# Kernel optimization log

Measured on AMD Instinct MI355X. Metric: run time of the kernel, lower is better.

The kernel has to match this reference:

```python
import jax, jax.numpy as jnp
import numpy as np

VOCAB = 128
HIDDEN = 1024

def setup_inputs() -> dict:
    key = jax.random.key(0)
    kx, ku, kw, kl, kb = jax.random.split(key, 5)
    B, S = 64, 512
    X = jax.random.randint(kx, (B, S), 0, VOCAB)
    # xavier_uniform bounds
    bu = float(np.sqrt(6.0 / (HIDDEN + HIDDEN)))
    bw = float(np.sqrt(6.0 / (HIDDEN + VOCAB)))
    U = jax.random.uniform(ku, (HIDDEN, HIDDEN), minval=-bu, maxval=bu, dtype=jnp.float32)
    W = jax.random.uniform(kw, (HIDDEN, VOCAB), minval=-bw, maxval=bw, dtype=jnp.float32)
    # nn.Linear(hidden, vocab): weight [vocab, hidden], bias [vocab]
    bl = float(1.0 / np.sqrt(HIDDEN))
    lin_w = jax.random.uniform(kl, (VOCAB, HIDDEN), minval=-bl, maxval=bl, dtype=jnp.float32)
    lin_b = jax.random.uniform(kb, (VOCAB,), minval=-bl, maxval=bl, dtype=jnp.float32)
    return {"X": X, "U": U, "W": W, "lin_w": lin_w, "lin_b": lin_b}

def reference(X, U, W, lin_w, lin_b):
    B, S = X.shape
    # one-hot embedding (use_embedding=False path)
    X_emb = jax.nn.one_hot(X, VOCAB, dtype=jnp.float32)  # [B,S,V]
    # precompute input contribution for all steps: x_t @ W.T -> [B,S,H]
    inp = jnp.einsum('bsv,hv->bsh', X_emb, W)
    h0 = jnp.zeros((B, HIDDEN), dtype=jnp.float32)

    def step(h, inp_t):
        h_new = jnp.tanh(h @ U.T + inp_t)  # [B,H]
        return h_new, h_new

    _, hs = jax.lax.scan(step, h0, jnp.swapaxes(inp, 0, 1))  # hs: [S,B,H]
    hs = jnp.swapaxes(hs, 0, 1)  # [B,S,H]
    logits = jnp.einsum('bsh,vh->bsv', hs, lin_w) + lin_b  # [B,S,V]
    return jax.nn.softmax(logits, axis=-1)
```

## Files before the change

kernel.cpp:

```cpp
#include <hip/hip_runtime.h>
#include <cstdint>

typedef float f32x4 __attribute__((ext_vector_type(4)));

static constexpr int Hdim = 1024;
static constexpr int Vdim = 128;
static constexpr int Bdim = 64;
static constexpr int Sdim = 512;

static constexpr int NB   = 8;
static constexpr int NI   = 32;
static constexpr int KCH  = 32;
static constexpr int SL   = 1028;
static constexpr int NBLK = 256;
static constexpr int BPC  = 32;
static constexpr int NCL  = 8;

__global__ void __launch_bounds__(256) pack_u_kernel(const float* __restrict__ U,
                                                     float* __restrict__ Up) {
  __shared__ float tile[32][257];
  const int s  = blockIdx.x;
  const int k0 = blockIdx.y * 256;
  const int t  = threadIdx.x;
  #pragma unroll
  for (int r = 0; r < 32; ++r)
    tile[r][t] = U[(size_t)(s * 32 + r) * Hdim + k0 + t];
  __syncthreads();
  const size_t base = ((size_t)s * Hdim + k0) * 32;
  #pragma unroll
  for (int r2 = 0; r2 < 32; ++r2) {
    int g = r2 * 256 + t;
    Up[base + g] = tile[g & 31][g >> 5];
  }
}

__global__ void transpose_w_kernel(const float* __restrict__ in, float* __restrict__ out) {
  __shared__ float tile[32][33];
  const int bx = blockIdx.x * 32;
  const int by = blockIdx.y * 32;
  const int tx = threadIdx.x, ty = threadIdx.y;
  #pragma unroll
  for (int dy = 0; dy < 32; dy += 8)
    tile[ty + dy][tx] = in[(size_t)(by + ty + dy) * Vdim + bx + tx];
  __syncthreads();
  #pragma unroll
  for (int dy = 0; dy < 32; dy += 8)
    out[(size_t)(bx + ty + dy) * Hdim + by + tx] = tile[tx][ty + dy];
}

__global__ void __launch_bounds__(256, 1) rnn_persist_kernel(
    const float* __restrict__ Up,
    const float* __restrict__ Wt,
    const int*   __restrict__ X,
    const float* __restrict__ lw,
    const float* __restrict__ lb,
    float* __restrict__ h0,
    float* __restrict__ h1,
    unsigned int* __restrict__ flags,
    float* __restrict__ out)
{
  __shared__ float hsm[NB * SL];
  __shared__ float part[4][NB][NI];
  __shared__ float partv[4][NB][4];

  const int tid  = threadIdx.x;
  const int blk  = blockIdx.x;
  const int cl   = blk >> 5;
  const int s    = blk & 31;
  const int i0   = s * NI;
  const int bg0  = cl * NB;
  const int kp   = tid >> 3;
  const int b    = tid & 7;
  const int w    = tid >> 6;
  const int lane = tid & 63;
  const float* Ublk = Up + (size_t)s * Hdim * NI;

  auto stage_h = [&](int t) {
    if (t == 0) {
      const f32x4 z = (f32x4){0.f, 0.f, 0.f, 0.f};
      #pragma unroll
      for (int r = 0; r < NB; ++r)
        *((f32x4*)&hsm[r * SL + tid * 4]) = z;
    } else {
      const float* hc = (t & 1) ? h1 : h0;
      const float* p = hc + (size_t)bg0 * Hdim + tid * 4;
      f32x4 v0, v1, v2, v3, v4, v5, v6, v7;
      asm volatile(
          "global_load_dwordx4 %0, %8, off sc0 sc1\n\t"
          "global_load_dwordx4 %1, %9, off sc0 sc1\n\t"
          "global_load_dwordx4 %2, %10, off sc0 sc1\n\t"
          "global_load_dwordx4 %3, %11, off sc0 sc1\n\t"
          "global_load_dwordx4 %4, %12, off sc0 sc1\n\t"
          "global_load_dwordx4 %5, %13, off sc0 sc1\n\t"
          "global_load_dwordx4 %6, %14, off sc0 sc1\n\t"
          "global_load_dwordx4 %7, %15, off sc0 sc1\n\t"
          "s_waitcnt vmcnt(0)"
          : "=&v"(v0), "=&v"(v1), "=&v"(v2), "=&v"(v3),
            "=&v"(v4), "=&v"(v5), "=&v"(v6), "=&v"(v7)
          : "v"(p), "v"(p + Hdim), "v"(p + 2 * Hdim), "v"(p + 3 * Hdim),
            "v"(p + 4 * Hdim), "v"(p + 5 * Hdim), "v"(p + 6 * Hdim), "v"(p + 7 * Hdim)
          : "memory");
      *((f32x4*)&hsm[0 * SL + tid * 4]) = v0;
      *((f32x4*)&hsm[1 * SL + tid * 4]) = v1;
      *((f32x4*)&hsm[2 * SL + tid * 4]) = v2;
      *((f32x4*)&hsm[3 * SL + tid * 4]) = v3;
      *((f32x4*)&hsm[4 * SL + tid * 4]) = v4;
      *((f32x4*)&hsm[5 * SL + tid * 4]) = v5;
      *((f32x4*)&hsm[6 * SL + tid * 4]) = v6;
      *((f32x4*)&hsm[7 * SL + tid * 4]) = v7;
    }
  };

  auto logits_partial = [&]() {
    float a0 = 0.f, a1 = 0.f, a2 = 0.f, a3 = 0.f;
    const f32x4* lw0 = (const f32x4*)(lw + (size_t)(4 * s)     * Hdim + kp * KCH);
    const f32x4* lw1 = (const f32x4*)(lw + (size_t)(4 * s + 1) * Hdim + kp * KCH);
    const f32x4* lw2 = (const f32x4*)(lw + (size_t)(4 * s + 2) * Hdim + kp * KCH);
    const f32x4* lw3 = (const f32x4*)(lw + (size_t)(4 * s + 3) * Hdim + kp * KCH);
    const f32x4* hr4 = (const f32x4*)&hsm[b * SL + kp * KCH];
    #pragma unroll
    for (int j = 0; j < KCH / 4; ++j) {
      int jj = (j + kp) & (KCH / 4 - 1);
      f32x4 hv = hr4[jj];
      f32x4 q0 = lw0[jj], q1 = lw1[jj], q2 = lw2[jj], q3 = lw3[jj];
      #pragma unroll
      for (int e = 0; e < 4; ++e) {
        a0 += hv[e] * q0[e]; a1 += hv[e] * q1[e];
        a2 += hv[e] * q2[e]; a3 += hv[e] * q3[e];
      }
    }
    #pragma unroll
    for (int d = 8; d < 64; d <<= 1) {
      a0 += __shfl_xor(a0, d, 64); a1 += __shfl_xor(a1, d, 64);
      a2 += __shfl_xor(a2, d, 64); a3 += __shfl_xor(a3, d, 64);
    }
    if ((lane & 56) == 0)
      *((f32x4*)&partv[w][b][0]) = (f32x4){a0, a1, a2, a3};
  };

  auto logits_combine = [&](int tt) {
    if (tid >= 128 && tid < 128 + 4 * NB) {
      const int q = tid - 128;
      const int bb = q >> 2, vv = q & 3;
      float lv = partv[0][bb][vv] + partv[1][bb][vv] + partv[2][bb][vv] + partv[3][bb][vv];
      lv += lb[4 * s + vv];
      out[((size_t)(bg0 + bb) * Sdim + tt) * Vdim + 4 * s + vv] = lv;
    }
  };

  for (int t = 0; t < Sdim; ++t) {
    stage_h(t);
    __syncthreads();

    {
      float acc[NI];
      #pragma unroll
      for (int i = 0; i < NI; ++i) acc[i] = 0.f;
      const float* hr = &hsm[b * SL + kp * KCH];
      const f32x4* ub = (const f32x4*)(Ublk + (size_t)kp * KCH * NI);
      #pragma unroll 4
      for (int j = 0; j < KCH; ++j) {
        int jj = (j + kp) & (KCH - 1);
        float hv = hr[jj];
        const f32x4* u = ub + (size_t)jj * (NI / 4);
        #pragma unroll
        for (int q = 0; q < NI / 4; ++q) {
          const f32x4 uq = u[q];
          acc[q * 4 + 0] += uq[0] * hv;
          acc[q * 4 + 1] += uq[1] * hv;
          acc[q * 4 + 2] += uq[2] * hv;
          acc[q * 4 + 3] += uq[3] * hv;
        }
      }
      #pragma unroll
      for (int i = 0; i < NI; ++i) {
        acc[i] += __shfl_xor(acc[i], 8, 64);
        acc[i] += __shfl_xor(acc[i], 16, 64);
        acc[i] += __shfl_xor(acc[i], 32, 64);
      }
      if ((lane & 56) == 0) {
        #pragma unroll
        for (int i = 0; i < NI; i += 4)
          *((f32x4*)&part[w][b][i]) = (f32x4){acc[i], acc[i + 1], acc[i + 2], acc[i + 3]};
      }
    }
    __syncthreads();

    {
      const int b2 = tid >> 5, i2 = tid & 31;
      float v = part[0][b2][i2] + part[1][b2][i2] + part[2][b2][i2] + part[3][b2][i2];
      const int x = X[(bg0 + b2) * Sdim + t];
      v += Wt[(size_t)x * Hdim + i0 + i2];
      v = tanhf(v);
      float* hn = (t & 1) ? h0 : h1;
      __hip_atomic_store(&hn[(size_t)(bg0 + b2) * Hdim + i0 + i2], v,
                         __ATOMIC_RELAXED, __HIP_MEMORY_SCOPE_SYSTEM);
    }

    asm volatile("s_waitcnt vmcnt(0)" ::: "memory");
    __syncthreads();
    if (tid == 0)
      __hip_atomic_store(&flags[cl * BPC + s], (unsigned)(t + 1),
                         __ATOMIC_RELAXED, __HIP_MEMORY_SCOPE_SYSTEM);

    if (t > 0) logits_partial();
    __syncthreads();
    if (t > 0) logits_combine(t - 1);

    if (tid < 64) {
      const unsigned int tag = (unsigned)(t + 1);
      unsigned int* f = &flags[cl * BPC + (tid & (BPC - 1))];
      while (true) {
        unsigned int fv = __hip_atomic_load(f, __ATOMIC_RELAXED, __HIP_MEMORY_SCOPE_SYSTEM);
        if (__all((int)(fv >= tag))) break;
        __builtin_amdgcn_s_sleep(1);
      }
    }
    __syncthreads();
  }

  stage_h(Sdim);
  __syncthreads();
  logits_partial();
  __syncthreads();
  logits_combine(Sdim - 1);
}

__global__ void __launch_bounds__(256) softmax_kernel(float* __restrict__ out) {
  const int row = blockIdx.x * 4 + (threadIdx.x >> 6);
  const int l = threadIdx.x & 63;
  float* rp = out + (size_t)row * Vdim;
  float2 v = *((const float2*)&rp[l * 2]);
  float m = fmaxf(v.x, v.y);
  #pragma unroll
  for (int d = 1; d < 64; d <<= 1) m = fmaxf(m, __shfl_xor(m, d, 64));
  float e0 = expf(v.x - m), e1 = expf(v.y - m);
  float ss = e0 + e1;
  #pragma unroll
  for (int d = 1; d < 64; d <<= 1) ss += __shfl_xor(ss, d, 64);
  const float inv = 1.f / ss;
  *((float2*)&rp[l * 2]) = make_float2(e0 * inv, e1 * inv);
}

extern "C" void kernel_launch(void* const* d_in, const int* in_sizes, int n_in,
                              void* d_out, int out_size, void* d_ws, size_t ws_size,
                              hipStream_t stream) {
  const int*   X  = (const int*)d_in[0];
  const float* U  = (const float*)d_in[1];
  const float* W  = (const float*)d_in[2];
  const float* lw = (const float*)d_in[3];
  const float* lb = (const float*)d_in[4];
  float* out = (float*)d_out;

  float* Up = (float*)d_ws;
  float* Wt = Up + (size_t)1024 * 1024;
  float* h0 = Wt + (size_t)128 * 1024;
  float* h1 = h0 + (size_t)64 * 1024;
  unsigned int* flags = (unsigned int*)(h1 + (size_t)64 * 1024);
  const size_t need = ((size_t)1024 * 1024 + 128 * 1024 + 2 * 64 * 1024) * 4 + NCL * BPC * 4;
  if (ws_size < need) return;

  hipMemsetAsync(flags, 0, (size_t)NCL * BPC * sizeof(unsigned int), stream);

  hipLaunchKernelGGL(pack_u_kernel, dim3(32, 4), dim3(256), 0, stream, U, Up);
  hipLaunchKernelGGL(transpose_w_kernel, dim3(4, 32), dim3(32, 8), 0, stream, W, Wt);

  void* args[] = {(void*)&Up, (void*)&Wt, (void*)&X, (void*)&lw, (void*)&lb,
                  (void*)&h0, (void*)&h1, (void*)&flags, (void*)&out};
  hipError_t ce = hipLaunchCooperativeKernel((void*)rnn_persist_kernel,
                                             dim3(NBLK), dim3(256), args, 0, stream);
  if (ce != hipSuccess) {
    hipLaunchKernelGGL(rnn_persist_kernel, dim3(NBLK), dim3(256), 0, stream,
                       Up, Wt, X, lw, lb, h0, h1, flags, out);
  }

  hipLaunchKernelGGL(softmax_kernel, dim3((Bdim * Sdim) / 4), dim3(256), 0, stream, out);
}
```

Baseline: 6.360 ms.

## Load hidden state directly into registers, drop LDS staging and a barrier

Each thread now loads its own 32-element slice of the previous hidden state straight from global memory into registers, instead of staging the full 8x1024 tile in shared memory and reading it back. This removes the LDS round trip and one __syncthreads per timestep. The logits partial is moved before the flag store, so another barrier goes away. In exchange, each thread issues uncoalesced-per-row loads where the same row data is shared across threads with different b, it holds 32 more registers, and the flag publish now waits for the logits work.

```diff
diff --git a/kernel.cpp b/kernel.cpp
--- a/kernel.cpp
+++ b/kernel.cpp
@@ -11,7 +11,6 @@
 static constexpr int NB   = 8;
 static constexpr int NI   = 32;
 static constexpr int KCH  = 32;
-static constexpr int SL   = 1028;
 static constexpr int NBLK = 256;
 static constexpr int BPC  = 32;
 static constexpr int NCL  = 8;
@@ -59,7 +58,6 @@
     unsigned int* __restrict__ flags,
     float* __restrict__ out)
 {
-  __shared__ float hsm[NB * SL];
   __shared__ float part[4][NB][NI];
   __shared__ float partv[4][NB][4];
 
@@ -75,39 +73,29 @@
   const int lane = tid & 63;
   const float* Ublk = Up + (size_t)s * Hdim * NI;
 
-  auto stage_h = [&](int t) {
+  f32x4 h4[8];
+
+  auto load_h = [&](int t) {
     if (t == 0) {
-      const f32x4 z = (f32x4){0.f, 0.f, 0.f, 0.f};
-      #pragma unroll
-      for (int r = 0; r < NB; ++r)
-        *((f32x4*)&hsm[r * SL + tid * 4]) = z;
+      #pragma unroll
+      for (int r = 0; r < 8; ++r) h4[r] = (f32x4){0.f, 0.f, 0.f, 0.f};
     } else {
       const float* hc = (t & 1) ? h1 : h0;
-      const float* p = hc + (size_t)bg0 * Hdim + tid * 4;
-      f32x4 v0, v1, v2, v3, v4, v5, v6, v7;
+      const float* p = hc + (size_t)(bg0 + b) * Hdim + kp * KCH;
       asm volatile(
           "global_load_dwordx4 %0, %8, off sc0 sc1\n\t"
-          "global_load_dwordx4 %1, %9, off sc0 sc1\n\t"
-          "global_load_dwordx4 %2, %10, off sc0 sc1\n\t"
-          "global_load_dwordx4 %3, %11, off sc0 sc1\n\t"
-          "global_load_dwordx4 %4, %12, off sc0 sc1\n\t"
-          "global_load_dwordx4 %5, %13, off sc0 sc1\n\t"
-          "global_load_dwordx4 %6, %14, off sc0 sc1\n\t"
-          "global_load_dwordx4 %7, %15, off sc0 sc1\n\t"
+          "global_load_dwordx4 %1, %8, off offset:16 sc0 sc1\n\t"
+          "global_load_dwordx4 %2, %8, off offset:32 sc0 sc1\n\t"
+          "global_load_dwordx4 %3, %8, off offset:48 sc0 sc1\n\t"
+          "global_load_dwordx4 %4, %8, off offset:64 sc0 sc1\n\t"
+          "global_load_dwordx4 %5, %8, off offset:80 sc0 sc1\n\t"
+          "global_load_dwordx4 %6, %8, off offset:96 sc0 sc1\n\t"
+          "global_load_dwordx4 %7, %8, off offset:112 sc0 sc1\n\t"
           "s_waitcnt vmcnt(0)"
-          : "=&v"(v0), "=&v"(v1), "=&v"(v2), "=&v"(v3),
-            "=&v"(v4), "=&v"(v5), "=&v"(v6), "=&v"(v7)
-          : "v"(p), "v"(p + Hdim), "v"(p + 2 * Hdim), "v"(p + 3 * Hdim),
-            "v"(p + 4 * Hdim), "v"(p + 5 * Hdim), "v"(p + 6 * Hdim), "v"(p + 7 * Hdim)
+          : "=&v"(h4[0]), "=&v"(h4[1]), "=&v"(h4[2]), "=&v"(h4[3]),
+            "=&v"(h4[4]), "=&v"(h4[5]), "=&v"(h4[6]), "=&v"(h4[7])
+          : "v"(p)
           : "memory");
-      *((f32x4*)&hsm[0 * SL + tid * 4]) = v0;
-      *((f32x4*)&hsm[1 * SL + tid * 4]) = v1;
-      *((f32x4*)&hsm[2 * SL + tid * 4]) = v2;
-      *((f32x4*)&hsm[3 * SL + tid * 4]) = v3;
-      *((f32x4*)&hsm[4 * SL + tid * 4]) = v4;
-      *((f32x4*)&hsm[5 * SL + tid * 4]) = v5;
-      *((f32x4*)&hsm[6 * SL + tid * 4]) = v6;
-      *((f32x4*)&hsm[7 * SL + tid * 4]) = v7;
     }
   };
 
@@ -117,12 +105,10 @@
     const f32x4* lw1 = (const f32x4*)(lw + (size_t)(4 * s + 1) * Hdim + kp * KCH);
     const f32x4* lw2 = (const f32x4*)(lw + (size_t)(4 * s + 2) * Hdim + kp * KCH);
     const f32x4* lw3 = (const f32x4*)(lw + (size_t)(4 * s + 3) * Hdim + kp * KCH);
-    const f32x4* hr4 = (const f32x4*)&hsm[b * SL + kp * KCH];
     #pragma unroll
-    for (int j = 0; j < KCH / 4; ++j) {
-      int jj = (j + kp) & (KCH / 4 - 1);
-      f32x4 hv = hr4[jj];
-      f32x4 q0 = lw0[jj], q1 = lw1[jj], q2 = lw2[jj], q3 = lw3[jj];
+    for (int j4 = 0; j4 < 8; ++j4) {
+      const f32x4 hv = h4[j4];
+      const f32x4 q0 = lw0[j4], q1 = lw1[j4], q2 = lw2[j4], q3 = lw3[j4];
       #pragma unroll
       for (int e = 0; e < 4; ++e) {
         a0 += hv[e] * q0[e]; a1 += hv[e] * q1[e];
@@ -149,27 +135,27 @@
   };
 
   for (int t = 0; t < Sdim; ++t) {
-    stage_h(t);
-    __syncthreads();
+    load_h(t);
 
     {
       float acc[NI];
       #pragma unroll
       for (int i = 0; i < NI; ++i) acc[i] = 0.f;
-      const float* hr = &hsm[b * SL + kp * KCH];
       const f32x4* ub = (const f32x4*)(Ublk + (size_t)kp * KCH * NI);
-      #pragma unroll 4
-      for (int j = 0; j < KCH; ++j) {
-        int jj = (j + kp) & (KCH - 1);
-        float hv = hr[jj];
-        const f32x4* u = ub + (size_t)jj * (NI / 4);
+      #pragma unroll
+      for (int j4 = 0; j4 < 8; ++j4) {
         #pragma unroll
-        for (int q = 0; q < NI / 4; ++q) {
-          const f32x4 uq = u[q];
-          acc[q * 4 + 0] += uq[0] * hv;
-          acc[q * 4 + 1] += uq[1] * hv;
-          acc[q * 4 + 2] += uq[2] * hv;
-          acc[q * 4 + 3] += uq[3] * hv;
+        for (int e = 0; e < 4; ++e) {
+          const float hv = h4[j4][e];
+          const f32x4* u = ub + (size_t)(j4 * 4 + e) * (NI / 4);
+          #pragma unroll
+          for (int q = 0; q < NI / 4; ++q) {
+            const f32x4 uq = u[q];
+            acc[q * 4 + 0] += uq[0] * hv;
+            acc[q * 4 + 1] += uq[1] * hv;
+            acc[q * 4 + 2] += uq[2] * hv;
+            acc[q * 4 + 3] += uq[3] * hv;
+          }
         }
       }
       #pragma unroll
@@ -197,14 +183,13 @@
                          __ATOMIC_RELAXED, __HIP_MEMORY_SCOPE_SYSTEM);
     }
 
+    if (t > 0) logits_partial();
+
     asm volatile("s_waitcnt vmcnt(0)" ::: "memory");
     __syncthreads();
     if (tid == 0)
       __hip_atomic_store(&flags[cl * BPC + s], (unsigned)(t + 1),
                          __ATOMIC_RELAXED, __HIP_MEMORY_SCOPE_SYSTEM);
-
-    if (t > 0) logits_partial();
-    __syncthreads();
     if (t > 0) logits_combine(t - 1);
 
     if (tid < 64) {
@@ -219,8 +204,7 @@
     __syncthreads();
   }
 
-  stage_h(Sdim);
-  __syncthreads();
+  load_h(Sdim);
   logits_partial();
   __syncthreads();
   logits_combine(Sdim - 1);
```

Measured after the change: 7.575 ms. 1.19x slower.

## Replace flag barrier with tagged value-plus-step packets for inter-block hidden state sync

Applied to the files above, without the earlier changes.

Each hidden value is now stored as a 64-bit packet holding the value and its step tag. Consumers spin on the hidden-state loads themselves until every tag matches, so the separate per-block flag store, the waitcnt, the extra __syncthreads and the flag-polling loop go away. This cuts a synchronization round trip per timestep. In exchange it doubles the hidden-state traffic, and every poll reloads a full 8-row tile, which may add memory pressure while spinning.

```diff
diff --git a/kernel.cpp b/kernel.cpp
--- a/kernel.cpp
+++ b/kernel.cpp
@@ -2,6 +2,7 @@
 #include <cstdint>
 
 typedef float f32x4 __attribute__((ext_vector_type(4)));
+typedef unsigned int u32x4 __attribute__((ext_vector_type(4)));
 
 static constexpr int Hdim = 1024;
 static constexpr int Vdim = 128;
@@ -54,9 +55,8 @@
     const int*   __restrict__ X,
     const float* __restrict__ lw,
     const float* __restrict__ lb,
-    float* __restrict__ h0,
-    float* __restrict__ h1,
-    unsigned int* __restrict__ flags,
+    unsigned int* __restrict__ hp0,
+    unsigned int* __restrict__ hp1,
     float* __restrict__ out)
 {
   __shared__ float hsm[NB * SL];
@@ -81,34 +81,56 @@
       #pragma unroll
       for (int r = 0; r < NB; ++r)
         *((f32x4*)&hsm[r * SL + tid * 4]) = z;
-    } else {
-      const float* hc = (t & 1) ? h1 : h0;
-      const float* p = hc + (size_t)bg0 * Hdim + tid * 4;
-      f32x4 v0, v1, v2, v3, v4, v5, v6, v7;
+      return;
+    }
+    const unsigned int* hc = (t & 1) ? hp1 : hp0;
+    const unsigned int* a0 = hc + ((size_t)(bg0 + 0) * Hdim + tid * 4) * 2;
+    const unsigned int* a1 = hc + ((size_t)(bg0 + 1) * Hdim + tid * 4) * 2;
+    const unsigned int* a2 = hc + ((size_t)(bg0 + 2) * Hdim + tid * 4) * 2;
+    const unsigned int* a3 = hc + ((size_t)(bg0 + 3) * Hdim + tid * 4) * 2;
+    const unsigned int* a4 = hc + ((size_t)(bg0 + 4) * Hdim + tid * 4) * 2;
+    const unsigned int* a5 = hc + ((size_t)(bg0 + 5) * Hdim + tid * 4) * 2;
+    const unsigned int* a6 = hc + ((size_t)(bg0 + 6) * Hdim + tid * 4) * 2;
+    const unsigned int* a7 = hc + ((size_t)(bg0 + 7) * Hdim + tid * 4) * 2;
+    const unsigned int tag = (unsigned int)t;
+    u32x4 q[16];
+    while (true) {
       asm volatile(
-          "global_load_dwordx4 %0, %8, off sc0 sc1\n\t"
-          "global_load_dwordx4 %1, %9, off sc0 sc1\n\t"
-          "global_load_dwordx4 %2, %10, off sc0 sc1\n\t"
-          "global_load_dwordx4 %3, %11, off sc0 sc1\n\t"
-          "global_load_dwordx4 %4, %12, off sc0 sc1\n\t"
-          "global_load_dwordx4 %5, %13, off sc0 sc1\n\t"
-          "global_load_dwordx4 %6, %14, off sc0 sc1\n\t"
-          "global_load_dwordx4 %7, %15, off sc0 sc1\n\t"
+          "global_load_dwordx4 %0, %16, off sc0 sc1\n\t"
+          "global_load_dwordx4 %1, %16, off offset:16 sc0 sc1\n\t"
+          "global_load_dwordx4 %2, %17, off sc0 sc1\n\t"
+          "global_load_dwordx4 %3, %17, off offset:16 sc0 sc1\n\t"
+          "global_load_dwordx4 %4, %18, off sc0 sc1\n\t"
+          "global_load_dwordx4 %5, %18, off offset:16 sc0 sc1\n\t"
+          "global_load_dwordx4 %6, %19, off sc0 sc1\n\t"
+          "global_load_dwordx4 %7, %19, off offset:16 sc0 sc1\n\t"
+          "global_load_dwordx4 %8, %20, off sc0 sc1\n\t"
+          "global_load_dwordx4 %9, %20, off offset:16 sc0 sc1\n\t"
+          "global_load_dwordx4 %10, %21, off sc0 sc1\n\t"
+          "global_load_dwordx4 %11, %21, off offset:16 sc0 sc1\n\t"
+          "global_load_dwordx4 %12, %22, off sc0 sc1\n\t"
+          "global_load_dwordx4 %13, %22, off offset:16 sc0 sc1\n\t"
+          "global_load_dwordx4 %14, %23, off sc0 sc1\n\t"
+          "global_load_dwordx4 %15, %23, off offset:16 sc0 sc1\n\t"
           "s_waitcnt vmcnt(0)"
-          : "=&v"(v0), "=&v"(v1), "=&v"(v2), "=&v"(v3),
-            "=&v"(v4), "=&v"(v5), "=&v"(v6), "=&v"(v7)
-          : "v"(p), "v"(p + Hdim), "v"(p + 2 * Hdim), "v"(p + 3 * Hdim),
-            "v"(p + 4 * Hdim), "v"(p + 5 * Hdim), "v"(p + 6 * Hdim), "v"(p + 7 * Hdim)
+          : "=&v"(q[0]), "=&v"(q[1]), "=&v"(q[2]), "=&v"(q[3]),
+            "=&v"(q[4]), "=&v"(q[5]), "=&v"(q[6]), "=&v"(q[7]),
+            "=&v"(q[8]), "=&v"(q[9]), "=&v"(q[10]), "=&v"(q[11]),
+            "=&v"(q[12]), "=&v"(q[13]), "=&v"(q[14]), "=&v"(q[15])
+          : "v"(a0), "v"(a1), "v"(a2), "v"(a3), "v"(a4), "v"(a5), "v"(a6), "v"(a7)
           : "memory");
-      *((f32x4*)&hsm[0 * SL + tid * 4]) = v0;
-      *((f32x4*)&hsm[1 * SL + tid * 4]) = v1;
-      *((f32x4*)&hsm[2 * SL + tid * 4]) = v2;
-      *((f32x4*)&hsm[3 * SL + tid * 4]) = v3;
-      *((f32x4*)&hsm[4 * SL + tid * 4]) = v4;
-      *((f32x4*)&hsm[5 * SL + tid * 4]) = v5;
-      *((f32x4*)&hsm[6 * SL + tid * 4]) = v6;
-      *((f32x4*)&hsm[7 * SL + tid * 4]) = v7;
-    }
+      unsigned int okb = 1u;
+      #pragma unroll
+      for (int i = 0; i < 16; ++i)
+        okb &= (unsigned)(q[i][1] == tag) & (unsigned)(q[i][3] == tag);
+      if (okb) break;
+      __builtin_amdgcn_s_sleep(1);
+    }
+    #pragma unroll
+    for (int r = 0; r < NB; ++r)
+      *((f32x4*)&hsm[r * SL + tid * 4]) = (f32x4){
+          __uint_as_float(q[2 * r][0]), __uint_as_float(q[2 * r][2]),
+          __uint_as_float(q[2 * r + 1][0]), __uint_as_float(q[2 * r + 1][2])};
   };
 
   auto logits_partial = [&]() {
@@ -192,31 +214,17 @@
       const int x = X[(bg0 + b2) * Sdim + t];
       v += Wt[(size_t)x * Hdim + i0 + i2];
       v = tanhf(v);
-      float* hn = (t & 1) ? h0 : h1;
-      __hip_atomic_store(&hn[(size_t)(bg0 + b2) * Hdim + i0 + i2], v,
-                         __ATOMIC_RELAXED, __HIP_MEMORY_SCOPE_SYSTEM);
-    }
-
-    asm volatile("s_waitcnt vmcnt(0)" ::: "memory");
-    __syncthreads();
-    if (tid == 0)
-      __hip_atomic_store(&flags[cl * BPC + s], (unsigned)(t + 1),
-                         __ATOMIC_RELAXED, __HIP_MEMORY_SCOPE_SYSTEM);
+      unsigned int* hn = (t & 1) ? hp0 : hp1;
+      unsigned int* hp = hn + ((size_t)(bg0 + b2) * Hdim + i0 + i2) * 2;
+      unsigned long long pkt = ((unsigned long long)(unsigned)(t + 1) << 32) |
+                               (unsigned long long)__float_as_uint(v);
+      asm volatile("global_store_dwordx2 %0, %1, off sc0 sc1"
+                   :: "v"(hp), "v"(pkt) : "memory");
+    }
 
     if (t > 0) logits_partial();
     __syncthreads();
     if (t > 0) logits_combine(t - 1);
-
-    if (tid < 64) {
-      const unsigned int tag = (unsigned)(t + 1);
-      unsigned int* f = &flags[cl * BPC + (tid & (BPC - 1))];
-      while (true) {
-        unsigned int fv = __hip_atomic_load(f, __ATOMIC_RELAXED, __HIP_MEMORY_SCOPE_SYSTEM);
-        if (__all((int)(fv >= tag))) break;
-        __builtin_amdgcn_s_sleep(1);
-      }
-    }
-    __syncthreads();
   }
 
   stage_h(Sdim);
@@ -254,24 +262,24 @@
 
   float* Up = (float*)d_ws;
   float* Wt = Up + (size_t)1024 * 1024;
-  float* h0 = Wt + (size_t)128 * 1024;
-  float* h1 = h0 + (size_t)64 * 1024;
-  unsigned int* flags = (unsigned int*)(h1 + (size_t)64 * 1024);
-  const size_t need = ((size_t)1024 * 1024 + 128 * 1024 + 2 * 64 * 1024) * 4 + NCL * BPC * 4;
+  unsigned int* hp0 = (unsigned int*)(Wt + (size_t)128 * 1024);
+  unsigned int* hp1 = hp0 + (size_t)Bdim * Hdim * 2;
+  const size_t need = ((size_t)1024 * 1024 + 128 * 1024) * 4 +
+                      (size_t)2 * Bdim * Hdim * 2 * 4;
   if (ws_size < need) return;
 
-  hipMemsetAsync(flags, 0, (size_t)NCL * BPC * sizeof(unsigned int), stream);
+  hipMemsetAsync(hp0, 0, (size_t)2 * Bdim * Hdim * 2 * sizeof(unsigned int), stream);
 
   hipLaunchKernelGGL(pack_u_kernel, dim3(32, 4), dim3(256), 0, stream, U, Up);
   hipLaunchKernelGGL(transpose_w_kernel, dim3(4, 32), dim3(32, 8), 0, stream, W, Wt);
 
   void* args[] = {(void*)&Up, (void*)&Wt, (void*)&X, (void*)&lw, (void*)&lb,
-                  (void*)&h0, (void*)&h1, (void*)&flags, (void*)&out};
+                  (void*)&hp0, (void*)&hp1, (void*)&out};
   hipError_t ce = hipLaunchCooperativeKernel((void*)rnn_persist_kernel,
                                              dim3(NBLK), dim3(256), args, 0, stream);
   if (ce != hipSuccess) {
     hipLaunchKernelGGL(rnn_persist_kernel, dim3(NBLK), dim3(256), 0, stream,
-                       Up, Wt, X, lw, lb, h0, h1, flags, out);
+                       Up, Wt, X, lw, lb, hp0, hp1, out);
   }
 
   hipLaunchKernelGGL(softmax_kernel, dim3((Bdim * Sdim) / 4), dim3(256), 0, stream, out);
```

New measurement: 6.503 ms. +2.3%, slower.

## Replace persistent flag-synchronised RNN kernel with one kernel launch per timestep

Applied to the files above, without the earlier changes.

The cooperative persistent kernel, which kept all 256 blocks resident and synchronised timesteps by polling system-scope flags, is replaced by one kernel launched per timestep, 513 launches in total. Each launch stages the previous hidden state from global memory with ordinary loads, does the recurrent matvec and the output-projection partial for the previous step, and writes the next hidden state. This removes the spin-waiting, the system-scope atomics and the cache-bypassing loads. In exchange every timestep pays a kernel launch and drain gap, and the per-block U slice is re-fetched on every launch.

```diff
diff --git a/kernel.cpp b/kernel.cpp
--- a/kernel.cpp
+++ b/kernel.cpp
@@ -13,8 +13,6 @@
 static constexpr int KCH  = 32;
 static constexpr int SL   = 1028;
 static constexpr int NBLK = 256;
-static constexpr int BPC  = 32;
-static constexpr int NCL  = 8;
 
 __global__ void __launch_bounds__(256) pack_u_kernel(const float* __restrict__ U,
                                                      float* __restrict__ Up) {
@@ -48,16 +46,16 @@
     out[(size_t)(bx + ty + dy) * Hdim + by + tx] = tile[tx][ty + dy];
 }
 
-__global__ void __launch_bounds__(256, 1) rnn_persist_kernel(
+__global__ void __launch_bounds__(256) rnn_step_kernel(
     const float* __restrict__ Up,
     const float* __restrict__ Wt,
     const int*   __restrict__ X,
     const float* __restrict__ lw,
     const float* __restrict__ lb,
-    float* __restrict__ h0,
-    float* __restrict__ h1,
-    unsigned int* __restrict__ flags,
-    float* __restrict__ out)
+    const float* __restrict__ hin,
+    float* __restrict__ hout,
+    float* __restrict__ out,
+    int t)
 {
   __shared__ float hsm[NB * SL];
   __shared__ float part[4][NB][NI];
@@ -75,43 +73,55 @@
   const int lane = tid & 63;
   const float* Ublk = Up + (size_t)s * Hdim * NI;
 
-  auto stage_h = [&](int t) {
-    if (t == 0) {
-      const f32x4 z = (f32x4){0.f, 0.f, 0.f, 0.f};
+  if (t == 0) {
+    const f32x4 z = (f32x4){0.f, 0.f, 0.f, 0.f};
+    #pragma unroll
+    for (int r = 0; r < NB; ++r)
+      *((f32x4*)&hsm[r * SL + tid * 4]) = z;
+  } else {
+    const f32x4* src = (const f32x4*)(hin + (size_t)bg0 * Hdim);
+    #pragma unroll
+    for (int r = 0; r < NB; ++r) {
+      f32x4 v = src[r * (Hdim / 4) + tid];
+      *((f32x4*)&hsm[r * SL + tid * 4]) = v;
+    }
+  }
+  __syncthreads();
+
+  if (t < Sdim) {
+    float acc[NI];
+    #pragma unroll
+    for (int i = 0; i < NI; ++i) acc[i] = 0.f;
+    const float* hr = &hsm[b * SL + kp * KCH];
+    const f32x4* ub = (const f32x4*)(Ublk + (size_t)kp * KCH * NI);
+    #pragma unroll 4
+    for (int j = 0; j < KCH; ++j) {
+      int jj = (j + kp) & (KCH - 1);
+      float hv = hr[jj];
+      const f32x4* u = ub + (size_t)jj * (NI / 4);
       #pragma unroll
-      for (int r = 0; r < NB; ++r)
-        *((f32x4*)&hsm[r * SL + tid * 4]) = z;
-    } else {
-      const float* hc = (t & 1) ? h1 : h0;
-      const float* p = hc + (size_t)bg0 * Hdim + tid * 4;
-      f32x4 v0, v1, v2, v3, v4, v5, v6, v7;
-      asm volatile(
-          "global_load_dwordx4 %0, %8, off sc0 sc1\n\t"
-          "global_load_dwordx4 %1, %9, off sc0 sc1\n\t"
-          "global_load_dwordx4 %2, %10, off sc0 sc1\n\t"
-          "global_load_dwordx4 %3, %11, off sc0 sc1\n\t"
-          "global_load_dwordx4 %4, %12, off sc0 sc1\n\t"
-          "global_load_dwordx4 %5, %13, off sc0 sc1\n\t"
-          "global_load_dwordx4 %6, %14, off sc0 sc1\n\t"
-          "global_load_dwordx4 %7, %15, off sc0 sc1\n\t"
-          "s_waitcnt vmcnt(0)"
-          : "=&v"(v0), "=&v"(v1), "=&v"(v2), "=&v"(v3),
-            "=&v"(v4), "=&v"(v5), "=&v"(v6), "=&v"(v7)
-          : "v"(p), "v"(p + Hdim), "v"(p + 2 * Hdim), "v"(p + 3 * Hdim),
-            "v"(p + 4 * Hdim), "v"(p + 5 * Hdim), "v"(p + 6 * Hdim), "v"(p + 7 * Hdim)
-          : "memory");
-      *((f32x4*)&hsm[0 * SL + tid * 4]) = v0;
-      *((f32x4*)&hsm[1 * SL + tid * 4]) = v1;
-      *((f32x4*)&hsm[2 * SL + tid * 4]) = v2;
-      *((f32x4*)&hsm[3 * SL + tid * 4]) = v3;
-      *((f32x4*)&hsm[4 * SL + tid * 4]) = v4;
-      *((f32x4*)&hsm[5 * SL + tid * 4]) = v5;
-      *((f32x4*)&hsm[6 * SL + tid * 4]) = v6;
-      *((f32x4*)&hsm[7 * SL + tid * 4]) = v7;
-    }
-  };
-
-  auto logits_partial = [&]() {
+      for (int q = 0; q < NI / 4; ++q) {
+        const f32x4 uq = u[q];
+        acc[q * 4 + 0] += uq[0] * hv;
+        acc[q * 4 + 1] += uq[1] * hv;
+        acc[q * 4 + 2] += uq[2] * hv;
+        acc[q * 4 + 3] += uq[3] * hv;
+      }
+    }
+    #pragma unroll
+    for (int i = 0; i < NI; ++i) {
+      acc[i] += __shfl_xor(acc[i], 8, 64);
+      acc[i] += __shfl_xor(acc[i], 16, 64);
+      acc[i] += __shfl_xor(acc[i], 32, 64);
+    }
+    if ((lane & 56) == 0) {
+      #pragma unroll
+      for (int i = 0; i < NI; i += 4)
+        *((f32x4*)&part[w][b][i]) = (f32x4){acc[i], acc[i + 1], acc[i + 2], acc[i + 3]};
+    }
+  }
+
+  if (t > 0) {
     float a0 = 0.f, a1 = 0.f, a2 = 0.f, a3 = 0.f;
     const f32x4* lw0 = (const f32x4*)(lw + (size_t)(4 * s)     * Hdim + kp * KCH);
     const f32x4* lw1 = (const f32x4*)(lw + (size_t)(4 * s + 1) * Hdim + kp * KCH);
@@ -136,94 +146,24 @@
     }
     if ((lane & 56) == 0)
       *((f32x4*)&partv[w][b][0]) = (f32x4){a0, a1, a2, a3};
-  };
-
-  auto logits_combine = [&](int tt) {
-    if (tid >= 128 && tid < 128 + 4 * NB) {
-      const int q = tid - 128;
-      const int bb = q >> 2, vv = q & 3;
-      float lv = partv[0][bb][vv] + partv[1][bb][vv] + partv[2][bb][vv] + partv[3][bb][vv];
-      lv += lb[4 * s + vv];
-      out[((size_t)(bg0 + bb) * Sdim + tt) * Vdim + 4 * s + vv] = lv;
-    }
-  };
-
-  for (int t = 0; t < Sdim; ++t) {
-    stage_h(t);
-    __syncthreads();
-
-    {
-      float acc[NI];
-      #pragma unroll
-      for (int i = 0; i < NI; ++i) acc[i] = 0.f;
-      const float* hr = &hsm[b * SL + kp * KCH];
-      const f32x4* ub = (const f32x4*)(Ublk + (size_t)kp * KCH * NI);
-      #pragma unroll 4
-      for (int j = 0; j < KCH; ++j) {
-        int jj = (j + kp) & (KCH - 1);
-        float hv = hr[jj];
-        const f32x4* u = ub + (size_t)jj * (NI / 4);
-        #pragma unroll
-        for (int q = 0; q < NI / 4; ++q) {
-          const f32x4 uq = u[q];
-          acc[q * 4 + 0] += uq[0] * hv;
-          acc[q * 4 + 1] += uq[1] * hv;
-          acc[q * 4 + 2] += uq[2] * hv;
-          acc[q * 4 + 3] += uq[3] * hv;
-        }
-      }
-      #pragma unroll
-      for (int i = 0; i < NI; ++i) {
-        acc[i] += __shfl_xor(acc[i], 8, 64);
-        acc[i] += __shfl_xor(acc[i], 16, 64);
-        acc[i] += __shfl_xor(acc[i], 32, 64);
-      }
-      if ((lane & 56) == 0) {
-        #pragma unroll
-        for (int i = 0; i < NI; i += 4)
-          *((f32x4*)&part[w][b][i]) = (f32x4){acc[i], acc[i + 1], acc[i + 2], acc[i + 3]};
-      }
-    }
-    __syncthreads();
-
-    {
-      const int b2 = tid >> 5, i2 = tid & 31;
-      float v = part[0][b2][i2] + part[1][b2][i2] + part[2][b2][i2] + part[3][b2][i2];
-      const int x = X[(bg0 + b2) * Sdim + t];
-      v += Wt[(size_t)x * Hdim + i0 + i2];
-      v = tanhf(v);
-      float* hn = (t & 1) ? h0 : h1;
-      __hip_atomic_store(&hn[(size_t)(bg0 + b2) * Hdim + i0 + i2], v,
-                         __ATOMIC_RELAXED, __HIP_MEMORY_SCOPE_SYSTEM);
-    }
-
-    asm volatile("s_waitcnt vmcnt(0)" ::: "memory");
-    __syncthreads();
-    if (tid == 0)
-      __hip_atomic_store(&flags[cl * BPC + s], (unsigned)(t + 1),
-                         __ATOMIC_RELAXED, __HIP_MEMORY_SCOPE_SYSTEM);
-
-    if (t > 0) logits_partial();
-    __syncthreads();
-    if (t > 0) logits_combine(t - 1);
-
-    if (tid < 64) {
-      const unsigned int tag = (unsigned)(t + 1);
-      unsigned int* f = &flags[cl * BPC + (tid & (BPC - 1))];
-      while (true) {
-        unsigned int fv = __hip_atomic_load(f, __ATOMIC_RELAXED, __HIP_MEMORY_SCOPE_SYSTEM);
-        if (__all((int)(fv >= tag))) break;
-        __builtin_amdgcn_s_sleep(1);
-      }
-    }
-    __syncthreads();
-  }
-
-  stage_h(Sdim);
-  __syncthreads();
-  logits_partial();
-  __syncthreads();
-  logits_combine(Sdim - 1);
+  }
+  __syncthreads();
+
+  if (t < Sdim) {
+    const int b2 = tid >> 5, i2 = tid & 31;
+    float v = part[0][b2][i2] + part[1][b2][i2] + part[2][b2][i2] + part[3][b2][i2];
+    const int x = X[(bg0 + b2) * Sdim + t];
+    v += Wt[(size_t)x * Hdim + i0 + i2];
+    hout[(size_t)(bg0 + b2) * Hdim + i0 + i2] = tanhf(v);
+  }
+
+  if (t > 0 && tid >= 128 && tid < 128 + 4 * NB) {
+    const int q = tid - 128;
+    const int bb = q >> 2, vv = q & 3;
+    float lv = partv[0][bb][vv] + partv[1][bb][vv] + partv[2][bb][vv] + partv[3][bb][vv];
+    lv += lb[4 * s + vv];
+    out[((size_t)(bg0 + bb) * Sdim + (t - 1)) * Vdim + 4 * s + vv] = lv;
+  }
 }
 
 __global__ void __launch_bounds__(256) softmax_kernel(float* __restrict__ out) {
@@ -256,22 +196,17 @@
   float* Wt = Up + (size_t)1024 * 1024;
   float* h0 = Wt + (size_t)128 * 1024;
   float* h1 = h0 + (size_t)64 * 1024;
-  unsigned int* flags = (unsigned int*)(h1 + (size_t)64 * 1024);
-  const size_t need = ((size_t)1024 * 1024 + 128 * 1024 + 2 * 64 * 1024) * 4 + NCL * BPC * 4;
+  const size_t need = ((size_t)1024 * 1024 + 128 * 1024 + 2 * 64 * 1024) * 4;
   if (ws_size < need) return;
-
-  hipMemsetAsync(flags, 0, (size_t)NCL * BPC * sizeof(unsigned int), stream);
 
   hipLaunchKernelGGL(pack_u_kernel, dim3(32, 4), dim3(256), 0, stream, U, Up);
   hipLaunchKernelGGL(transpose_w_kernel, dim3(4, 32), dim3(32, 8), 0, stream, W, Wt);
 
-  void* args[] = {(void*)&Up, (void*)&Wt, (void*)&X, (void*)&lw, (void*)&lb,
-                  (void*)&h0, (void*)&h1, (void*)&flags, (void*)&out};
-  hipError_t ce = hipLaunchCooperativeKernel((void*)rnn_persist_kernel,
-                                             dim3(NBLK), dim3(256), args, 0, stream);
-  if (ce != hipSuccess) {
-    hipLaunchKernelGGL(rnn_persist_kernel, dim3(NBLK), dim3(256), 0, stream,
-                       Up, Wt, X, lw, lb, h0, h1, flags, out);
+  for (int t = 0; t <= Sdim; ++t) {
+    const float* hin = (t & 1) ? h1 : h0;
+    float* hout      = (t & 1) ? h0 : h1;
+    hipLaunchKernelGGL(rnn_step_kernel, dim3(NBLK), dim3(256), 0, stream,
+                       Up, Wt, X, lw, lb, hin, hout, out, t);
   }
 
   hipLaunchKernelGGL(softmax_kernel, dim3((Bdim * Sdim) / 4), dim3(256), 0, stream, out);
```

New measurement: 6.244 ms. Within noise of the previous version (-1.8%).
